# Optimization experiments

Hardware: AMD Instinct MI355X
Metric: run time of the kernel (lower is better)

## Reference

```python
import jax, jax.numpy as jnp
import numpy as np
import math

B, S, DIM = 2, 2048, 4096
N_HEADS, N_KV = 32, 8
HD = DIM // N_HEADS           # 128
N_REP = N_HEADS // N_KV       # 4
MAX_SEQ = 2048


def _rope_freqs(seq_len, head_dim):
    inv = 1.0 / (10000.0 ** (np.arange(0, head_dim, 2, dtype=np.float32) / head_dim))
    ang = np.outer(np.arange(seq_len, dtype=np.float32), inv)  # [S, HD/2]
    return jnp.asarray(np.cos(ang)), jnp.asarray(np.sin(ang))


def setup_inputs() -> dict:
    key = jax.random.key(0)
    ks = jax.random.split(key, 5)
    x = jax.random.normal(ks[0], (B, S, DIM), dtype=jnp.float32)
    wq = jax.random.normal(ks[1], (DIM, N_HEADS * HD), dtype=jnp.float32) * 0.02
    wk = jax.random.normal(ks[2], (DIM, N_KV * HD), dtype=jnp.float32) * 0.02
    wv = jax.random.normal(ks[3], (DIM, N_KV * HD), dtype=jnp.float32) * 0.02
    wo = jax.random.normal(ks[4], (N_HEADS * HD, DIM), dtype=jnp.float32) * 0.02
    freqs_cos, freqs_sin = _rope_freqs(S, HD)
    return {"x": x, "wq": wq, "wk": wk, "wv": wv, "wo": wo,
            "freqs_cos": freqs_cos, "freqs_sin": freqs_sin, "start_pos": 0}


def _apply_rope(t, cos, sin):
    # t: [B, S, H, HD]; adjacent pairs (2i, 2i+1) form complex numbers
    tr = t.reshape(*t.shape[:-1], HD // 2, 2)
    xr, xi = tr[..., 0], tr[..., 1]
    c = cos[None, :, None, :]  # [1, S, 1, HD/2]
    s = sin[None, :, None, :]
    o = jnp.stack([xr * c - xi * s, xr * s + xi * c], axis=-1)
    return o.reshape(t.shape)


def reference(x, wq, wk, wv, wo, freqs_cos, freqs_sin, start_pos):
    batch, seq_len, _ = x.shape
    q = (x @ wq).reshape(batch, seq_len, N_HEADS, HD)
    k = (x @ wk).reshape(batch, seq_len, N_KV, HD)
    v = (x @ wv).reshape(batch, seq_len, N_KV, HD)
    xq = _apply_rope(q, freqs_cos, freqs_sin)
    xk = _apply_rope(k, freqs_cos, freqs_sin)

    # KV-cache append (buffer initialized to zeros, as in the module)
    cache_k = jnp.zeros((batch, MAX_SEQ, N_KV, HD), dtype=x.dtype)
    cache_v = jnp.zeros((batch, MAX_SEQ, N_KV, HD), dtype=x.dtype)
    cache_k = jax.lax.dynamic_update_slice(cache_k, xk, (0, start_pos, 0, 0))
    cache_v = jax.lax.dynamic_update_slice(cache_v, v, (0, start_pos, 0, 0))
    keys = cache_k[:, : start_pos + seq_len]    # [B, T, KV, HD]
    values = cache_v[:, : start_pos + seq_len]

    # GQA: repeat kv heads n_rep times
    keys = jnp.repeat(keys, N_REP, axis=2)      # [B, T, H, HD]
    values = jnp.repeat(values, N_REP, axis=2)

    # [B, H, Sq, T] scores; no causal mask, matching the original module
    scores = jnp.einsum("bqhd,bkhd->bhqk", xq, keys) / math.sqrt(HD)
    attn = jax.nn.softmax(scores, axis=-1)
    out = jnp.einsum("bhqk,bkhd->bqhd", attn, values)
    out = out.reshape(batch, seq_len, N_HEADS * HD)
    return out @ wo
```

## Files before the change

kernel.cpp:

```cpp
#include <hip/hip_runtime.h>

#define S_LEN 2048

typedef __bf16 bf16x8 __attribute__((ext_vector_type(8)));
typedef float f32x4 __attribute__((ext_vector_type(4)));

static __device__ __forceinline__ unsigned short f32_to_bf16(float f){
  unsigned int u = __float_as_uint(f);
  u += 0x7FFFu + ((u >> 16) & 1u);
  return (unsigned short)(u >> 16);
}
static __device__ __forceinline__ float bf16_to_f32(unsigned short h){
  return __uint_as_float(((unsigned int)h) << 16);
}
static __device__ __forceinline__ bf16x8 ld_bf16x8(const unsigned short* p){
  return *reinterpret_cast<const bf16x8*>(p);
}
static __device__ __forceinline__ void async_copy16(const void* g, void* l){
  __builtin_amdgcn_global_load_lds(
      (const __attribute__((address_space(1))) void*)g,
      (__attribute__((address_space(3))) void*)l, 16, 0, 0);
}

__global__ void conv_f32_bf16(const float* __restrict__ in, unsigned short* __restrict__ out, int n4){
  int i = blockIdx.x * 256 + threadIdx.x;
  if (i >= n4) return;
  float4 v = ((const float4*)in)[i];
  ushort4 o;
  o.x = f32_to_bf16(v.x); o.y = f32_to_bf16(v.y);
  o.z = f32_to_bf16(v.z); o.w = f32_to_bf16(v.w);
  ((ushort4*)out)[i] = o;
}

__global__ void transpose_w(const float* __restrict__ in, unsigned short* __restrict__ out, int K, int N){
  __shared__ float tile[32][33];
  int n0 = blockIdx.x * 32, k0 = blockIdx.y * 32;
  int tx = threadIdx.x, ty = threadIdx.y;
  #pragma unroll
  for (int i=0;i<4;++i)
    tile[ty + i*8][tx] = in[(size_t)(k0 + ty + i*8) * N + n0 + tx];
  __syncthreads();
  #pragma unroll
  for (int i=0;i<4;++i)
    out[(size_t)(n0 + ty + i*8) * K + k0 + tx] = f32_to_bf16(tile[tx][ty + i*8]);
}

__global__ void transpose_v(const unsigned short* __restrict__ in, unsigned short* __restrict__ out){
  __shared__ unsigned short tile[32][33];
  int r0 = blockIdx.x * 32;
  int c0 = blockIdx.y * 32;
  int tx = threadIdx.x, ty = threadIdx.y;
  #pragma unroll
  for (int i=0;i<4;++i)
    tile[ty + i*8][tx] = in[(size_t)(r0 + ty + i*8) * 6144 + 5120 + c0 + tx];
  __syncthreads();
  #pragma unroll
  for (int i=0;i<4;++i)
    out[(size_t)(c0 + ty + i*8) * 4096 + r0 + tx] = tile[tx][ty + i*8];
}

__global__ void rope_inplace(unsigned short* __restrict__ t, const float* __restrict__ cs,
                             const float* __restrict__ sn, int heads, float scale){
  int idx = blockIdx.x * 256 + threadIdx.x;
  int j = idx & 63;
  int tmp = idx >> 6;
  int h = tmp & (heads - 1);
  int row = tmp / heads;
  int s = row & (S_LEN - 1);
  float c = cs[s*64 + j], si = sn[s*64 + j];
  size_t base = (size_t)row * 6144 + (h << 7) + (j << 1);
  float xr = bf16_to_f32(t[base]);
  float xi = bf16_to_f32(t[base + 1]);
  t[base]     = f32_to_bf16((xr * c - xi * si) * scale);
  t[base + 1] = f32_to_bf16((xr * si + xi * c) * scale);
}

#define MFMA16 __builtin_amdgcn_mfma_f32_16x16x32_bf16
#define GBAR()   asm volatile("s_barrier" ::: "memory")
#define LGKM0()  do { asm volatile("s_waitcnt lgkmcnt(0)" ::: "memory"); \
                      __builtin_amdgcn_sched_barrier(0); } while(0)
#define VMW(N)   asm volatile("s_waitcnt vmcnt(" #N ")" ::: "memory")
#define STG(gp, lp) do { \
    async_copy16((gp),             (lp) + wofs); \
    async_copy16((gp) + (Ks<<6),   (lp) + 4096 + wofs); \
  } while(0)

static __device__ __forceinline__ void read_a4(bf16x8 (&a)[4][2], const unsigned short* base, int s0, int s1){
  #pragma unroll
  for (int m=0;m<4;++m){
    const unsigned short* p = base + m*1024;
    a[m][0] = ld_bf16x8(p + s0);
    a[m][1] = ld_bf16x8(p + s1);
  }
}
template<int NO>
static __device__ __forceinline__ void read_b2(bf16x8 (&b)[4][2], const unsigned short* base, int s0, int s1){
  #pragma unroll
  for (int n=0;n<2;++n){
    const unsigned short* p = base + (NO+n)*1024;
    b[NO+n][0] = ld_bf16x8(p + s0);
    b[NO+n][1] = ld_bf16x8(p + s1);
  }
}
template<int MO, int NO>
static __device__ __forceinline__ void mfma_quad(f32x4 (&acc)[8][4], const bf16x8 (&a)[4][2], const bf16x8 (&b)[4][2]){
  __builtin_amdgcn_s_setprio(1);
  #pragma unroll
  for (int ks=0; ks<2; ++ks)
    #pragma unroll
    for (int m=0;m<4;++m)
      #pragma unroll
      for (int n=0;n<2;++n)
        acc[MO+m][NO+n] = MFMA16(a[m][ks], b[NO+n][ks], acc[MO+m][NO+n], 0, 0, 0);
  __builtin_amdgcn_s_setprio(0);
}

template<bool OUT_BF16>
__global__ __launch_bounds__(512, 2) void gemm256_bt(
    const unsigned short* __restrict__ A,
    const unsigned short* __restrict__ Bt,
    void* __restrict__ Cout, int N, int K)
{
  __shared__ alignas(16) unsigned short sm[65536];
  unsigned short* A0 = sm;
  unsigned short* B0 = sm + 16384;
  unsigned short* A1 = sm + 32768;
  unsigned short* B1 = sm + 49152;

  const int tid  = threadIdx.x;
  const int wave = tid >> 6;
  const int lane = tid & 63;
  const int lm = lane & 15;
  const int kq = lane >> 4;
  const int wm = wave >> 2;
  const int wn = wave & 3;
  const int wofs = wave * 512;
  const int srow = wave * 8 + (lane >> 3);
  const int scol = ((lane & 7) ^ (lane >> 3)) * 8;
  const int s0 = (kq ^ (lm & 7)) * 8;
  const int s1 = s0 ^ 32;

  const size_t Ks = (size_t)K;
  const size_t bm = (size_t)blockIdx.y * 256;
  const size_t bn = (size_t)blockIdx.x * 256;
  const unsigned short* Asrc = A  + (bm + srow) * Ks + scol;
  const unsigned short* Bsrc = Bt + (bn + srow) * Ks + scol;
  const size_t h1 = (size_t)128 * Ks;

  const int ardo = (wm*128 + lm) * 64;
  const int brdo = (wn*64  + lm) * 64;

  const f32x4 zero4 = {0.f,0.f,0.f,0.f};
  f32x4 acc[8][4];
  #pragma unroll
  for (int i=0;i<8;++i)
    #pragma unroll
    for (int j=0;j<4;++j) acc[i][j] = zero4;
  bf16x8 a[4][2], b[4][2];

  const int NT = K >> 6;

  STG(Bsrc,           B0);
  STG(Bsrc + h1,      B0 + 8192);
  STG(Asrc,           A0);
  STG(Asrc + h1,      A0 + 8192);
  STG(Bsrc + 64,      B1);
  STG(Bsrc + h1 + 64, B1 + 8192);
  VMW(4);
  GBAR();

  for (int it = 0; it < (NT >> 1); ++it){
    const int k1 = (2*it + 1) * 64;
    const int k2 = ((2*it + 2) & (NT - 1)) * 64;
    const int k3 = ((2*it + 3) & (NT - 1)) * 64;
    read_a4(a, A0 + ardo, s0, s1);
    read_b2<0>(b, B0 + brdo, s0, s1);
    STG(Asrc + k1, A1);
    GBAR(); LGKM0(); mfma_quad<0,0>(acc, a, b); GBAR();
    read_b2<2>(b, B0 + brdo, s0, s1);
    STG(Asrc + h1 + k1, A1 + 8192);
    GBAR(); LGKM0(); mfma_quad<0,2>(acc, a, b); GBAR();
    read_a4(a, A0 + ardo + 4096, s0, s1);
    STG(Bsrc + k2, B0);
    GBAR(); LGKM0(); mfma_quad<4,0>(acc, a, b); GBAR();
    STG(Bsrc + h1 + k2, B0 + 8192);
    VMW(4);
    GBAR(); LGKM0(); mfma_quad<4,2>(acc, a, b); GBAR();
    read_a4(a, A1 + ardo, s0, s1);
    read_b2<0>(b, B1 + brdo, s0, s1);
    STG(Asrc + k2, A0);
    GBAR(); LGKM0(); mfma_quad<0,0>(acc, a, b); GBAR();
    read_b2<2>(b, B1 + brdo, s0, s1);
    STG(Asrc + h1 + k2, A0 + 8192);
    GBAR(); LGKM0(); mfma_quad<0,2>(acc, a, b); GBAR();
    read_a4(a, A1 + ardo + 4096, s0, s1);
    STG(Bsrc + k3, B1);
    GBAR(); LGKM0(); mfma_quad<4,0>(acc, a, b); GBAR();
    STG(Bsrc + h1 + k3, B1 + 8192);
    VMW(4);
    GBAR(); LGKM0(); mfma_quad<4,2>(acc, a, b); GBAR();
  }
  VMW(0);

  #pragma unroll
  for (int mi=0; mi<8; ++mi){
    const size_t row = bm + wm*128 + mi*16 + kq*4;
    #pragma unroll
    for (int ni=0; ni<4; ++ni){
      const size_t col = bn + wn*64 + ni*16 + lm;
      #pragma unroll
      for (int r=0; r<4; ++r){
        if constexpr (OUT_BF16)
          ((unsigned short*)Cout)[(row + r) * N + col] = f32_to_bf16(acc[mi][ni][r]);
        else
          ((float*)Cout)[(row + r) * N + col] = acc[mi][ni][r];
      }
    }
  }
}

#define PP 72
#define QKV_STRIDE 6144

__global__ __launch_bounds__(256, 2) void flash_attn(
    const unsigned short* __restrict__ QKV,
    const unsigned short* __restrict__ VT,
    unsigned short* __restrict__ O)
{
  __shared__ alignas(16) unsigned short Ksm[64 * 128];
  __shared__ alignas(16) unsigned short VTsm[128 * 64];
  __shared__ alignas(16) unsigned short Psm[4 * 32 * PP];

  const int tid  = threadIdx.x;
  const int wave = tid >> 6;
  const int lane = tid & 63;
  const int lm = lane & 15;
  const int kq = lane >> 4;
  const int b   = blockIdx.z;
  const int h   = blockIdx.y;
  const int kvh = h >> 2;
  const int q0  = blockIdx.x * 128;

  bf16x8 qf[2][4];
  #pragma unroll
  for (int mt=0; mt<2; ++mt){
    const size_t qbase = (size_t)(b * S_LEN + q0 + mt*64 + wave*16 + lm) * QKV_STRIDE + h * 128;
    #pragma unroll
    for (int kf=0; kf<4; ++kf)
      qf[mt][kf] = ld_bf16x8(&QKV[qbase + kf*32 + kq*8]);
  }

  const f32x4 zero4 = {0.f,0.f,0.f,0.f};
  f32x4 Oacc[2][8];
  #pragma unroll
  for (int mt=0; mt<2; ++mt)
    #pragma unroll
    for (int i=0;i<8;++i) Oacc[mt][i] = zero4;
  f32x4 lacc[2] = {zero4, zero4};

  union { unsigned short s[8]; bf16x8 v; } ou;
  #pragma unroll
  for (int i=0;i<8;++i) ou.s[i] = 0x3F80;
  const bf16x8 ones = ou.v;

  const unsigned short* Kg = QKV + 4096 + (size_t)kvh * 128 + (size_t)b * S_LEN * QKV_STRIDE;
  const unsigned short* Vg = VT + (size_t)kvh * 128 * 4096 + (size_t)b * S_LEN;
  unsigned short* Pw = &Psm[wave * 32 * PP];

  const int kkey_in = lane >> 4;
  const int kccp    = lane & 15;
  const int vd_in   = lane >> 3;
  const int vchl    = ((lane & 7) ^ (vd_in & 7)) * 8;

  for (int kt = 0; kt < S_LEN/64; ++kt){
    #pragma unroll
    for (int c=0;c<4;++c){
      int kb4 = (wave*4 + c) * 4;
      int key = kb4 + kkey_in;
      int ccl = kccp ^ (key & 7);
      async_copy16(Kg + (size_t)(kt*64 + key) * QKV_STRIDE + ccl*8, &Ksm[kb4 * 128]);
    }
    #pragma unroll
    for (int c=0;c<4;++c){
      int d0 = (wave*4 + c) * 8;
      int d  = d0 + vd_in;
      async_copy16(Vg + (size_t)d * 4096 + kt*64 + vchl, &VTsm[d0 * 64]);
    }
    __syncthreads();

    f32x4 sacc[2][4];
    #pragma unroll
    for (int nt=0;nt<4;++nt){ sacc[0][nt] = zero4; sacc[1][nt] = zero4; }
    #pragma unroll
    for (int nt=0; nt<4; ++nt){
      const int n = nt*16 + lm;
      #pragma unroll
      for (int kf=0; kf<4; ++kf){
        int pc = ((kf*4 + kq) ^ (lm & 7)) * 8;
        bf16x8 kfrag = ld_bf16x8(&Ksm[n*128 + pc]);
        sacc[0][nt] = __builtin_amdgcn_mfma_f32_16x16x32_bf16(qf[0][kf], kfrag, sacc[0][nt], 0,0,0);
        sacc[1][nt] = __builtin_amdgcn_mfma_f32_16x16x32_bf16(qf[1][kf], kfrag, sacc[1][nt], 0,0,0);
      }
    }

    #pragma unroll
    for (int mt=0; mt<2; ++mt){
      #pragma unroll
      for (int nt=0; nt<4; ++nt){
        #pragma unroll
        for (int e=0; e<4; ++e){
          float p = __expf(sacc[mt][nt][e]);
          Pw[(mt*16 + kq*4 + e)*PP + nt*16 + lm] = f32_to_bf16(p);
        }
      }
    }

    #pragma unroll
    for (int kf2=0; kf2<2; ++kf2){
      bf16x8 pf0 = ld_bf16x8(&Pw[(     lm)*PP + kf2*32 + kq*8]);
      bf16x8 pf1 = ld_bf16x8(&Pw[(16 + lm)*PP + kf2*32 + kq*8]);
      lacc[0] = __builtin_amdgcn_mfma_f32_16x16x32_bf16(pf0, ones, lacc[0], 0,0,0);
      lacc[1] = __builtin_amdgcn_mfma_f32_16x16x32_bf16(pf1, ones, lacc[1], 0,0,0);
      #pragma unroll
      for (int dt=0; dt<8; ++dt){
        int pc = ((kf2*4 + kq) ^ (lm & 7)) * 8;
        bf16x8 vfr = ld_bf16x8(&VTsm[(dt*16 + lm)*64 + pc]);
        Oacc[0][dt] = __builtin_amdgcn_mfma_f32_16x16x32_bf16(pf0, vfr, Oacc[0][dt], 0,0,0);
        Oacc[1][dt] = __builtin_amdgcn_mfma_f32_16x16x32_bf16(pf1, vfr, Oacc[1][dt], 0,0,0);
      }
    }
    __syncthreads();
  }

  #pragma unroll
  for (int mt=0; mt<2; ++mt){
    float inv[4];
    #pragma unroll
    for (int r=0;r<4;++r) inv[r] = __builtin_amdgcn_rcpf(lacc[mt][r]);
    const size_t obase = (((size_t)(b * S_LEN + q0 + mt*64 + wave*16 + kq*4)) * 32 + h) * 128;
    #pragma unroll
    for (int r=0;r<4;++r){
      #pragma unroll
      for (int dt=0; dt<8; ++dt)
        O[obase + (size_t)r * 4096 + dt*16 + lm] = f32_to_bf16(Oacc[mt][dt][r] * inv[r]);
    }
  }
}

extern "C" void kernel_launch(void* const* d_in, const int* in_sizes, int n_in,
                              void* d_out, int out_size, void* d_ws, size_t ws_size,
                              hipStream_t stream)
{
  const float* x    = (const float*)d_in[0];
  const float* wq   = (const float*)d_in[1];
  const float* wk   = (const float*)d_in[2];
  const float* wv   = (const float*)d_in[3];
  const float* wo   = (const float*)d_in[4];
  const float* fcos = (const float*)d_in[5];
  const float* fsin = (const float*)d_in[6];

  float* out = (float*)d_out;
  char* w = (char*)d_ws;
  const size_t MB = 1ull << 20;
  unsigned short* xb    = (unsigned short*)(w + 0);
  unsigned short* wqkvT = (unsigned short*)(w + 32*MB);
  unsigned short* woT   = (unsigned short*)(w + 80*MB);
  unsigned short* qkv   = (unsigned short*)(w + 112*MB);
  unsigned short* vT    = (unsigned short*)(w + 32*MB);
  unsigned short* attn  = (unsigned short*)(w + 0);

  conv_f32_bf16<<<dim3(16384), dim3(256), 0, stream>>>(x, xb, 4194304);

  transpose_w<<<dim3(128,128), dim3(32,8), 0, stream>>>(wq, wqkvT,                      4096, 4096);
  transpose_w<<<dim3(32,128),  dim3(32,8), 0, stream>>>(wk, wqkvT + (size_t)4096*4096, 4096, 1024);
  transpose_w<<<dim3(32,128),  dim3(32,8), 0, stream>>>(wv, wqkvT + (size_t)5120*4096, 4096, 1024);
  transpose_w<<<dim3(128,128), dim3(32,8), 0, stream>>>(wo, woT, 4096, 4096);

  gemm256_bt<true><<<dim3(24,16), dim3(512), 0, stream>>>(xb, wqkvT, qkv, 6144, 4096);

  rope_inplace<<<dim3(32768), dim3(256), 0, stream>>>(qkv,        fcos, fsin, 32, 0.08838834764831845f);
  rope_inplace<<<dim3(8192),  dim3(256), 0, stream>>>(qkv + 4096, fcos, fsin, 8, 1.0f);

  transpose_v<<<dim3(128,32), dim3(32,8), 0, stream>>>(qkv, vT);

  flash_attn<<<dim3(16, 32, 2), dim3(256), 0, stream>>>(qkv, vT, attn);

  gemm256_bt<false><<<dim3(16,16), dim3(512), 0, stream>>>(attn, woT, out, 4096, 4096);
}
```

Before: 737.7 us.

## Double-buffer flash attention, XCD-swizzle GEMMs, split QKV GEMM, vectorize RoPE

Flash attention now runs 512-thread blocks covering 256 queries, with double-buffered K/V tiles in LDS, prefetch of the next tile overlapped with compute, and s_setprio around the MFMA phases. The QKV projection is split into a 256-tile GEMM for Q and a new 128-tile GEMM for K/V, which removes the partial-wave grid of 24x16 blocks. All GEMMs and attention remap block IDs with an XCD swizzle so that neighbouring tiles land on the same die for L2 reuse. RoPE reads and writes each pair as one 32-bit word. The risks are the extra launch, a simple single-buffered 128 GEMM, and lower occupancy in attention.

New measurement: 748.6 us. About the same (+1.5%).

```diff
diff --git a/kernel.cpp b/kernel.cpp
--- a/kernel.cpp
+++ b/kernel.cpp
@@ -21,6 +21,19 @@
       (const __attribute__((address_space(1))) void*)g,
       (__attribute__((address_space(3))) void*)l, 16, 0, 0);
 }
+
+#define MFMA16 __builtin_amdgcn_mfma_f32_16x16x32_bf16
+#define GBAR()   asm volatile("s_barrier" ::: "memory")
+#define LGKM0()  do { asm volatile("s_waitcnt lgkmcnt(0)" ::: "memory"); \
+                      __builtin_amdgcn_sched_barrier(0); } while(0)
+#define VMW(N)   asm volatile("s_waitcnt vmcnt(" #N ")" ::: "memory")
+
+#define XCD_SWZ(bxv, byv) \
+  int flat_ = blockIdx.y * gridDim.x + blockIdx.x; \
+  const int cpx_ = (gridDim.x * gridDim.y) >> 3; \
+  flat_ = (flat_ & 7) * cpx_ + (flat_ >> 3); \
+  const int bxv = flat_ % gridDim.x; \
+  const int byv = flat_ / gridDim.x;
 
 __global__ void conv_f32_bf16(const float* __restrict__ in, unsigned short* __restrict__ out, int n4){
   int i = blockIdx.x * 256 + threadIdx.x;
@@ -69,17 +82,14 @@
   int s = row & (S_LEN - 1);
   float c = cs[s*64 + j], si = sn[s*64 + j];
   size_t base = (size_t)row * 6144 + (h << 7) + (j << 1);
-  float xr = bf16_to_f32(t[base]);
-  float xi = bf16_to_f32(t[base + 1]);
-  t[base]     = f32_to_bf16((xr * c - xi * si) * scale);
-  t[base + 1] = f32_to_bf16((xr * si + xi * c) * scale);
-}
-
-#define MFMA16 __builtin_amdgcn_mfma_f32_16x16x32_bf16
-#define GBAR()   asm volatile("s_barrier" ::: "memory")
-#define LGKM0()  do { asm volatile("s_waitcnt lgkmcnt(0)" ::: "memory"); \
-                      __builtin_amdgcn_sched_barrier(0); } while(0)
-#define VMW(N)   asm volatile("s_waitcnt vmcnt(" #N ")" ::: "memory")
+  unsigned int pr = *reinterpret_cast<const unsigned int*>(&t[base]);
+  float xr = bf16_to_f32((unsigned short)(pr & 0xFFFFu));
+  float xi = bf16_to_f32((unsigned short)(pr >> 16));
+  unsigned int lo = f32_to_bf16((xr * c - xi * si) * scale);
+  unsigned int hi = f32_to_bf16((xr * si + xi * c) * scale);
+  *reinterpret_cast<unsigned int*>(&t[base]) = lo | (hi << 16);
+}
+
 #define STG(gp, lp) do { \
     async_copy16((gp),             (lp) + wofs); \
     async_copy16((gp) + (Ks<<6),   (lp) + 4096 + wofs); \
@@ -140,9 +150,10 @@
   const int s0 = (kq ^ (lm & 7)) * 8;
   const int s1 = s0 ^ 32;
 
+  XCD_SWZ(bxx, byy);
   const size_t Ks = (size_t)K;
-  const size_t bm = (size_t)blockIdx.y * 256;
-  const size_t bn = (size_t)blockIdx.x * 256;
+  const size_t bm = (size_t)byy * 256;
+  const size_t bn = (size_t)bxx * 256;
   const unsigned short* Asrc = A  + (bm + srow) * Ks + scol;
   const unsigned short* Bsrc = Bt + (bn + srow) * Ks + scol;
   const size_t h1 = (size_t)128 * Ks;
@@ -219,17 +230,95 @@
   }
 }
 
+template<bool OUT_BF16>
+__global__ __launch_bounds__(256, 2) void gemm128_bt(
+    const unsigned short* __restrict__ A,
+    const unsigned short* __restrict__ Bt,
+    void* __restrict__ Cout, int N, int K)
+{
+  __shared__ alignas(16) unsigned short Asm[128 * 32];
+  __shared__ alignas(16) unsigned short Bsm[128 * 32];
+  const int tid  = threadIdx.x;
+  const int wave = tid >> 6;
+  const int lane = tid & 63;
+  const int lm = lane & 15;
+  const int kq = lane >> 4;
+  const int wm = (wave >> 1) * 64;
+  const int wn = (wave & 1) * 64;
+  XCD_SWZ(bxx, byy);
+  const size_t bm = (size_t)byy * 128;
+  const size_t bn = (size_t)bxx * 128;
+
+  const f32x4 zero4 = {0.f, 0.f, 0.f, 0.f};
+  f32x4 acc[4][4];
+  #pragma unroll
+  for (int i=0;i<4;++i)
+    #pragma unroll
+    for (int j=0;j<4;++j) acc[i][j] = zero4;
+
+  const int srow = lane >> 2;
+  const int sc   = ((lane & 3) ^ ((lane >> 3) & 3)) * 8;
+  const unsigned short* gA0 = A  + (bm + wave*32      + srow) * (size_t)K + sc;
+  const unsigned short* gA1 = A  + (bm + wave*32 + 16 + srow) * (size_t)K + sc;
+  const unsigned short* gB0 = Bt + (bn + wave*32      + srow) * (size_t)K + sc;
+  const unsigned short* gB1 = Bt + (bn + wave*32 + 16 + srow) * (size_t)K + sc;
+  unsigned short* lA0 = &Asm[(wave*32     ) * 32];
+  unsigned short* lA1 = &Asm[(wave*32 + 16) * 32];
+  unsigned short* lB0 = &Bsm[(wave*32     ) * 32];
+  unsigned short* lB1 = &Bsm[(wave*32 + 16) * 32];
+
+  const int p8 = (kq ^ ((lm >> 1) & 3)) * 8;
+
+  for (int k0 = 0; k0 < K; k0 += 32){
+    async_copy16(gA0, lA0);
+    async_copy16(gA1, lA1);
+    async_copy16(gB0, lB0);
+    async_copy16(gB1, lB1);
+    gA0 += 32; gA1 += 32; gB0 += 32; gB1 += 32;
+    __syncthreads();
+
+    bf16x8 af[4], bfr[4];
+    #pragma unroll
+    for (int i=0;i<4;++i){
+      af[i]  = ld_bf16x8(&Asm[(wm + i*16 + lm)*32 + p8]);
+      bfr[i] = ld_bf16x8(&Bsm[(wn + i*16 + lm)*32 + p8]);
+    }
+    #pragma unroll
+    for (int mi=0; mi<4; ++mi)
+      #pragma unroll
+      for (int ni=0; ni<4; ++ni)
+        acc[mi][ni] = MFMA16(af[mi], bfr[ni], acc[mi][ni], 0, 0, 0);
+    __syncthreads();
+  }
+
+  #pragma unroll
+  for (int mi=0; mi<4; ++mi){
+    #pragma unroll
+    for (int ni=0; ni<4; ++ni){
+      #pragma unroll
+      for (int r=0; r<4; ++r){
+        size_t row = bm + wm + mi*16 + kq*4 + r;
+        size_t col = bn + wn + ni*16 + lm;
+        if constexpr (OUT_BF16)
+          ((unsigned short*)Cout)[row * N + col] = f32_to_bf16(acc[mi][ni][r]);
+        else
+          ((float*)Cout)[row * N + col] = acc[mi][ni][r];
+      }
+    }
+  }
+}
+
 #define PP 72
 #define QKV_STRIDE 6144
 
-__global__ __launch_bounds__(256, 2) void flash_attn(
+__global__ __launch_bounds__(512, 1) void flash_attn(
     const unsigned short* __restrict__ QKV,
     const unsigned short* __restrict__ VT,
     unsigned short* __restrict__ O)
 {
-  __shared__ alignas(16) unsigned short Ksm[64 * 128];
-  __shared__ alignas(16) unsigned short VTsm[128 * 64];
-  __shared__ alignas(16) unsigned short Psm[4 * 32 * PP];
+  __shared__ alignas(16) unsigned short Ksm[2][64 * 128];
+  __shared__ alignas(16) unsigned short VTsm[2][128 * 64];
+  __shared__ alignas(16) unsigned short Psm[8 * 32 * PP];
 
   const int tid  = threadIdx.x;
   const int wave = tid >> 6;
@@ -237,14 +326,14 @@
   const int lm = lane & 15;
   const int kq = lane >> 4;
   const int b   = blockIdx.z;
-  const int h   = blockIdx.y;
+  XCD_SWZ(qb, h);
   const int kvh = h >> 2;
-  const int q0  = blockIdx.x * 128;
+  const int q0  = qb * 256;
 
   bf16x8 qf[2][4];
   #pragma unroll
   for (int mt=0; mt<2; ++mt){
-    const size_t qbase = (size_t)(b * S_LEN + q0 + mt*64 + wave*16 + lm) * QKV_STRIDE + h * 128;
+    const size_t qbase = (size_t)(b * S_LEN + q0 + wave*32 + mt*16 + lm) * QKV_STRIDE + h * 128;
     #pragma unroll
     for (int kf=0; kf<4; ++kf)
       qf[mt][kf] = ld_bf16x8(&QKV[qbase + kf*32 + kq*8]);
@@ -272,36 +361,53 @@
   const int vd_in   = lane >> 3;
   const int vchl    = ((lane & 7) ^ (vd_in & 7)) * 8;
 
-  for (int kt = 0; kt < S_LEN/64; ++kt){
-    #pragma unroll
-    for (int c=0;c<4;++c){
-      int kb4 = (wave*4 + c) * 4;
+  auto stage = [&](int kt, int buf) {
+    unsigned short* Kd = Ksm[buf];
+    unsigned short* Vd = VTsm[buf];
+    #pragma unroll
+    for (int c=0;c<2;++c){
+      int kb4 = (wave*2 + c) * 4;
       int key = kb4 + kkey_in;
       int ccl = kccp ^ (key & 7);
-      async_copy16(Kg + (size_t)(kt*64 + key) * QKV_STRIDE + ccl*8, &Ksm[kb4 * 128]);
-    }
-    #pragma unroll
-    for (int c=0;c<4;++c){
-      int d0 = (wave*4 + c) * 8;
+      async_copy16(Kg + (size_t)(kt*64 + key) * QKV_STRIDE + ccl*8, Kd + kb4*128);
+    }
+    #pragma unroll
+    for (int c=0;c<2;++c){
+      int d0 = (wave*2 + c) * 8;
       int d  = d0 + vd_in;
-      async_copy16(Vg + (size_t)d * 4096 + kt*64 + vchl, &VTsm[d0 * 64]);
-    }
-    __syncthreads();
+      async_copy16(Vg + (size_t)d * 4096 + kt*64 + vchl, Vd + d0*64);
+    }
+  };
+
+  stage(0, 0);
+  for (int kt = 0; kt < S_LEN/64; ++kt){
+    const int cur = kt & 1;
+    if (kt + 1 < S_LEN/64){
+      stage(kt + 1, cur ^ 1);
+      VMW(4);
+    } else {
+      VMW(0);
+    }
+    GBAR();
+    const unsigned short* Kc = Ksm[cur];
+    const unsigned short* Vc = VTsm[cur];
 
     f32x4 sacc[2][4];
     #pragma unroll
     for (int nt=0;nt<4;++nt){ sacc[0][nt] = zero4; sacc[1][nt] = zero4; }
+    __builtin_amdgcn_s_setprio(1);
     #pragma unroll
     for (int nt=0; nt<4; ++nt){
       const int n = nt*16 + lm;
       #pragma unroll
       for (int kf=0; kf<4; ++kf){
         int pc = ((kf*4 + kq) ^ (lm & 7)) * 8;
-        bf16x8 kfrag = ld_bf16x8(&Ksm[n*128 + pc]);
-        sacc[0][nt] = __builtin_amdgcn_mfma_f32_16x16x32_bf16(qf[0][kf], kfrag, sacc[0][nt], 0,0,0);
-        sacc[1][nt] = __builtin_amdgcn_mfma_f32_16x16x32_bf16(qf[1][kf], kfrag, sacc[1][nt], 0,0,0);
+        bf16x8 kfrag = ld_bf16x8(&Kc[n*128 + pc]);
+        sacc[0][nt] = MFMA16(qf[0][kf], kfrag, sacc[0][nt], 0,0,0);
+        sacc[1][nt] = MFMA16(qf[1][kf], kfrag, sacc[1][nt], 0,0,0);
       }
     }
+    __builtin_amdgcn_s_setprio(0);
 
     #pragma unroll
     for (int mt=0; mt<2; ++mt){
@@ -315,21 +421,23 @@
       }
     }
 
+    __builtin_amdgcn_s_setprio(1);
     #pragma unroll
     for (int kf2=0; kf2<2; ++kf2){
       bf16x8 pf0 = ld_bf16x8(&Pw[(     lm)*PP + kf2*32 + kq*8]);
       bf16x8 pf1 = ld_bf16x8(&Pw[(16 + lm)*PP + kf2*32 + kq*8]);
-      lacc[0] = __builtin_amdgcn_mfma_f32_16x16x32_bf16(pf0, ones, lacc[0], 0,0,0);
-      lacc[1] = __builtin_amdgcn_mfma_f32_16x16x32_bf16(pf1, ones, lacc[1], 0,0,0);
+      lacc[0] = MFMA16(pf0, ones, lacc[0], 0,0,0);
+      lacc[1] = MFMA16(pf1, ones, lacc[1], 0,0,0);
       #pragma unroll
       for (int dt=0; dt<8; ++dt){
         int pc = ((kf2*4 + kq) ^ (lm & 7)) * 8;
-        bf16x8 vfr = ld_bf16x8(&VTsm[(dt*16 + lm)*64 + pc]);
-        Oacc[0][dt] = __builtin_amdgcn_mfma_f32_16x16x32_bf16(pf0, vfr, Oacc[0][dt], 0,0,0);
-        Oacc[1][dt] = __builtin_amdgcn_mfma_f32_16x16x32_bf16(pf1, vfr, Oacc[1][dt], 0,0,0);
+        bf16x8 vfr = ld_bf16x8(&Vc[(dt*16 + lm)*64 + pc]);
+        Oacc[0][dt] = MFMA16(pf0, vfr, Oacc[0][dt], 0,0,0);
+        Oacc[1][dt] = MFMA16(pf1, vfr, Oacc[1][dt], 0,0,0);
       }
     }
-    __syncthreads();
+    __builtin_amdgcn_s_setprio(0);
+    GBAR();
   }
 
   #pragma unroll
@@ -337,7 +445,7 @@
     float inv[4];
     #pragma unroll
     for (int r=0;r<4;++r) inv[r] = __builtin_amdgcn_rcpf(lacc[mt][r]);
-    const size_t obase = (((size_t)(b * S_LEN + q0 + mt*64 + wave*16 + kq*4)) * 32 + h) * 128;
+    const size_t obase = (((size_t)(b * S_LEN + q0 + wave*32 + mt*16 + kq*4)) * 32 + h) * 128;
     #pragma unroll
     for (int r=0;r<4;++r){
       #pragma unroll
@@ -376,14 +484,16 @@
   transpose_w<<<dim3(32,128),  dim3(32,8), 0, stream>>>(wv, wqkvT + (size_t)5120*4096, 4096, 1024);
   transpose_w<<<dim3(128,128), dim3(32,8), 0, stream>>>(wo, woT, 4096, 4096);
 
-  gemm256_bt<true><<<dim3(24,16), dim3(512), 0, stream>>>(xb, wqkvT, qkv, 6144, 4096);
+  gemm256_bt<true><<<dim3(16,16), dim3(512), 0, stream>>>(xb, wqkvT, qkv, 6144, 4096);
+  gemm128_bt<true><<<dim3(16,32), dim3(256), 0, stream>>>(
+      xb, wqkvT + (size_t)4096*4096, qkv + 4096, 6144, 4096);
 
   rope_inplace<<<dim3(32768), dim3(256), 0, stream>>>(qkv,        fcos, fsin, 32, 0.08838834764831845f);
   rope_inplace<<<dim3(8192),  dim3(256), 0, stream>>>(qkv + 4096, fcos, fsin, 8, 1.0f);
 
   transpose_v<<<dim3(128,32), dim3(32,8), 0, stream>>>(qkv, vT);
 
-  flash_attn<<<dim3(16, 32, 2), dim3(256), 0, stream>>>(qkv, vT, attn);
+  flash_attn<<<dim3(8, 32, 2), dim3(512), 0, stream>>>(qkv, vT, attn);
 
   gemm256_bt<false><<<dim3(16,16), dim3(512), 0, stream>>>(attn, woT, out, 4096, 4096);
 }
```
